# Performance work log

Hardware: AMD Instinct MI355X
Metric: run time of the kernel (lower is better)

## Reference

```python
import jax, jax.numpy as jnp
import numpy as np

# dims
C = 256; G = 16; GC = C // G; K = 3; P = K * K
N, H, W = 8, 56, 56
HID = int(C * 4.0)
PAD = 1; STRIDE = 1; DIL = 1
OFFSET_SCALE = 1.0
LN_EPS = 1e-6


def setup_inputs() -> dict:
    key = jax.random.key(0)
    ks = jax.random.split(key, 16)
    rn = lambda k, shape, s: jax.random.normal(k, shape, jnp.float32) * s
    return {
        "x": rn(ks[0], (N, H, W, C), 1.0),
        "norm1_g": jnp.ones((C,), jnp.float32), "norm1_b": jnp.zeros((C,), jnp.float32),
        "norm2_g": jnp.ones((C,), jnp.float32), "norm2_b": jnp.zeros((C,), jnp.float32),
        "gamma1": jnp.ones((C,), jnp.float32), "gamma2": jnp.ones((C,), jnp.float32),
        "dw_w": rn(ks[1], (C, 1, K, K), 0.1), "dw_b": rn(ks[2], (C,), 0.02),
        "dwln_g": jnp.ones((C,), jnp.float32), "dwln_b": jnp.zeros((C,), jnp.float32),
        "off_w": rn(ks[3], (C, G * P * 2), 0.01), "off_b": rn(ks[4], (G * P * 2,), 0.01),
        "mask_w": rn(ks[5], (C, G * P), 0.02), "mask_b": rn(ks[6], (G * P,), 0.02),
        "in_w": rn(ks[7], (C, C), C ** -0.5), "in_b": jnp.zeros((C,), jnp.float32),
        "out_w": rn(ks[8], (C, C), C ** -0.5), "out_b": jnp.zeros((C,), jnp.float32),
        "fc1_w": rn(ks[9], (C, HID), C ** -0.5), "fc1_b": jnp.zeros((HID,), jnp.float32),
        "fc2_w": rn(ks[10], (HID, C), HID ** -0.5), "fc2_b": jnp.zeros((C,), jnp.float32),
    }


def layer_norm(x, g, b):
    mu = x.mean(-1, keepdims=True)
    var = ((x - mu) ** 2).mean(-1, keepdims=True)
    return (x - mu) * jax.lax.rsqrt(var + LN_EPS) * g + b


def depthwise_conv(x, w, b):
    # x: (N,H,W,C), w: (C,1,K,K) depthwise
    y = jax.lax.conv_general_dilated(
        x.transpose(0, 3, 1, 2), w, (1, 1), ((PAD, PAD), (PAD, PAD)),
        feature_group_count=C)
    return y.transpose(0, 2, 3, 1) + b


def bilinear_gather(img, gx, gy):
    # img: (Hp,Wp,GC); gx,gy: (L,) normalized grid coords in [-1,1]
    # F.grid_sample(mode='bilinear', padding_mode='zeros', align_corners=False)
    Hp, Wp = img.shape[0], img.shape[1]
    x = (gx + 1.0) * 0.5 * Wp - 0.5
    y = (gy + 1.0) * 0.5 * Hp - 0.5
    x0 = jnp.floor(x); y0 = jnp.floor(y)
    lx = x - x0; ly = y - y0

    def tap(yi, xi, wgt):
        valid = (yi >= 0) & (yi < Hp) & (xi >= 0) & (xi < Wp)
        yc = jnp.clip(yi, 0, Hp - 1).astype(jnp.int32)
        xc = jnp.clip(xi, 0, Wp - 1).astype(jnp.int32)
        return jnp.where(valid, wgt, 0.0)[:, None] * img[yc, xc]  # (L,GC)

    return (tap(y0, x0, (1 - lx) * (1 - ly)) + tap(y0, x0 + 1, lx * (1 - ly))
            + tap(y0 + 1, x0, (1 - lx) * ly) + tap(y0 + 1, x0 + 1, lx * ly))


def dcnv3(xin, dw_w, dw_b, dwln_g, dwln_b, off_w, off_b, mask_w, mask_b,
          in_w, in_b, out_w, out_b):
    # xin: (N,H,W,C)
    xproj = xin @ in_w + in_b
    x1 = depthwise_conv(xin, dw_w, dw_b)
    x1 = jax.nn.gelu(layer_norm(x1, dwln_g, dwln_b), approximate=False)
    offset = x1 @ off_w + off_b                                   # (N,H,W,G*P*2)
    mask = jax.nn.softmax((x1 @ mask_w + mask_b).reshape(N, H, W, G, P), axis=-1)

    xp = jnp.pad(xproj, ((0, 0), (PAD, PAD), (PAD, PAD), (0, 0)))
    Hp, Wp = H + 2 * PAD, W + 2 * PAD

    # reference points, normalized by padded spatial shape; last dim = (x,y)
    base = (DIL * (K - 1)) // 2 + 0.5
    ref_y = (base + jnp.arange(H, dtype=jnp.float32) * STRIDE) / Hp
    ref_x = (base + jnp.arange(W, dtype=jnp.float32) * STRIDE) / Wp
    ref = jnp.stack(jnp.broadcast_arrays(ref_x[None, :], ref_y[:, None]), -1)  # (H,W,2)

    # dilation grid, x-major flatten order (torch meshgrid 'ij' on (x,y))
    lin = -float((DIL * (K - 1)) // 2) + jnp.arange(K, dtype=jnp.float32) * DIL
    gx, gy = jnp.meshgrid(lin, lin, indexing='ij')  # gx varies along dim0
    gridpts = jnp.stack([gx / Wp, gy / Hp], -1).reshape(P, 2)

    off = offset.reshape(N, H, W, G, P, 2) * OFFSET_SCALE / jnp.array([Wp, Hp], jnp.float32)
    loc = (ref[None, :, :, None, None, :] + gridpts[None, None, None, None, :, :] * OFFSET_SCALE
           + off)                                                 # (N,H,W,G,P,2)
    sg = 2.0 * loc - 1.0

    # per-group images and sampling grids
    img = xp.reshape(N, Hp, Wp, G, GC).transpose(0, 3, 1, 2, 4).reshape(N * G, Hp, Wp, GC)
    gxs = sg[..., 0].transpose(0, 3, 1, 2, 4).reshape(N * G, H * W * P)
    gys = sg[..., 1].transpose(0, 3, 1, 2, 4).reshape(N * G, H * W * P)
    sampled = jax.vmap(bilinear_gather)(img, gxs, gys)            # (N*G, H*W*P, GC)
    sampled = sampled.reshape(N, G, H, W, P, GC)

    out = jnp.einsum('nghwpc,nhwgp->nhwgc', sampled, mask).reshape(N, H, W, C)
    return out @ out_w + out_b


def reference(x, norm1_g, norm1_b, norm2_g, norm2_b, gamma1, gamma2,
              dw_w, dw_b, dwln_g, dwln_b, off_w, off_b, mask_w, mask_b,
              in_w, in_b, out_w, out_b, fc1_w, fc1_b, fc2_w, fc2_b):
    h = dcnv3(layer_norm(x, norm1_g, norm1_b), dw_w, dw_b, dwln_g, dwln_b,
              off_w, off_b, mask_w, mask_b, in_w, in_b, out_w, out_b)
    x = x + gamma1 * h
    m = jax.nn.gelu(layer_norm(x, norm2_g, norm2_b) @ fc1_w + fc1_b,
                    approximate=False) @ fc2_w + fc2_b
    return x + gamma2 * m
```

## Files before the change

kernel.cpp:

```cpp
#include <hip/hip_runtime.h>
#include <math.h>

#define NB 8
#define HH 56
#define WWD 56
#define CC 256
#define PIX (NB*HH*WWD)

typedef __attribute__((ext_vector_type(8))) short bf16x8;
typedef __attribute__((ext_vector_type(8))) unsigned short u16x8;
typedef __attribute__((ext_vector_type(4))) float f32x4;

__device__ __forceinline__ float gelu_fast(float x) {
    float z = x * fmaf(0.0713554668f, x*x, 1.5957691216f);
    return x * __fdividef(1.0f, 1.0f + __expf(-z));
}
__device__ __forceinline__ unsigned short f2bf(float f) {
    unsigned u = __float_as_uint(f);
    unsigned r = (u + 0x7fffu + ((u >> 16) & 1u)) >> 16;
    return (unsigned short)r;
}
__device__ __forceinline__ float bf2f(unsigned short b) {
    return __uint_as_float(((unsigned)b) << 16);
}
__device__ __forceinline__ void gl_lds16(const void* g, void* l) {
    __builtin_amdgcn_global_load_lds(
        (const __attribute__((address_space(1))) void*)g,
        (__attribute__((address_space(3))) void*)l, 16, 0, 0);
}
__device__ __forceinline__ void wave_reduce2(float& s, float& sq) {
    #pragma unroll
    for (int o = 32; o >= 1; o >>= 1) {
        s  += __shfl_xor(s, o);
        sq += __shfl_xor(sq, o);
    }
}

__global__ __launch_bounds__(256) void prep_kernel(
    const float* __restrict__ inw, const float* __restrict__ offw,
    const float* __restrict__ offb, const float* __restrict__ mskw,
    const float* __restrict__ mskb, const float* __restrict__ outw,
    const float* __restrict__ f1w, const float* __restrict__ f2w,
    const float* __restrict__ dww,
    unsigned short* __restrict__ bt_in, unsigned short* __restrict__ bt_om,
    unsigned short* __restrict__ bt_out, unsigned short* __restrict__ bt_fc1,
    unsigned short* __restrict__ bt_fc2, float* __restrict__ wt9,
    float* __restrict__ bias_om)
{
    int i = blockIdx.x * 256 + threadIdx.x;
    if (i < 65536) {
        int n = i >> 8, k = i & 255;
        bt_in[i] = f2bf(inw[(size_t)k*256 + n]);
    } else if (i < 196608) {
        int j = i - 65536;
        int n = j >> 8, k = j & 255;
        float v = (n < 288) ? offw[(size_t)k*288 + n]
                : (n < 432) ? mskw[(size_t)k*144 + (n-288)] : 0.f;
        bt_om[j] = f2bf(v);
    } else if (i < 262144) {
        int j = i - 196608;
        int n = j >> 8, k = j & 255;
        bt_out[j] = f2bf(outw[(size_t)k*256 + n]);
    } else if (i < 524288) {
        int j = i - 262144;
        int n = j >> 8, k = j & 255;
        bt_fc1[j] = f2bf(f1w[(size_t)k*1024 + n]);
    } else if (i < 786432) {
        int j = i - 524288;
        int n = j >> 10, k = j & 1023;
        bt_fc2[j] = f2bf(f2w[(size_t)k*256 + n]);
    } else if (i < 788736) {
        int j = i - 786432;
        int t = j >> 8, c = j & 255;
        wt9[j] = dww[(size_t)c*9 + t];
    } else if (i < 789248) {
        int j = i - 788736;
        bias_om[j] = (j < 288) ? offb[j] : (j < 432) ? mskb[j-288] : 0.f;
    }
}

__global__ __launch_bounds__(256) void ln_bf_kernel(
    const float* __restrict__ in, const float* __restrict__ g,
    const float* __restrict__ b, unsigned short* __restrict__ out)
{
    int wave = threadIdx.x >> 6, lane = threadIdx.x & 63;
    int pix = blockIdx.x * 4 + wave;
    int c0 = lane * 4;
    float4 v = *reinterpret_cast<const float4*>(&in[(size_t)pix * CC + c0]);
    float s = v.x + v.y + v.z + v.w;
    float sq = v.x*v.x + v.y*v.y + v.z*v.z + v.w*v.w;
    wave_reduce2(s, sq);
    float mu = s * (1.0f/256.0f);
    float var = sq * (1.0f/256.0f) - mu*mu;
    float rs = rsqrtf(var + 1e-6f);
    float4 gv = *reinterpret_cast<const float4*>(&g[c0]);
    float4 bv = *reinterpret_cast<const float4*>(&b[c0]);
    ushort4 o;
    o.x = f2bf((v.x-mu)*rs*gv.x + bv.x);
    o.y = f2bf((v.y-mu)*rs*gv.y + bv.y);
    o.z = f2bf((v.z-mu)*rs*gv.z + bv.z);
    o.w = f2bf((v.w-mu)*rs*gv.w + bv.w);
    *reinterpret_cast<ushort4*>(&out[(size_t)pix * CC + c0]) = o;
}

__global__ __launch_bounds__(256) void dwconv_ln_gelu_kernel(
    const unsigned short* __restrict__ xl, const float* __restrict__ wt9,
    const float* __restrict__ cb, const float* __restrict__ lg,
    const float* __restrict__ lb, unsigned short* __restrict__ out)
{
    int bid = blockIdx.x;
    int wg = (bid & 7) * (gridDim.x >> 3) + (bid >> 3);
    int wave = threadIdx.x >> 6, lane = threadIdx.x & 63;
    int pix0 = wg * 16 + wave * 4;
    int n = pix0 / (HH*WWD); int rem = pix0 % (HH*WWD);
    int h = rem / WWD, wb = rem % WWD;
    int c0 = lane * 4;

    float4 wv[9];
    #pragma unroll
    for (int t = 0; t < 9; ++t)
        wv[t] = *reinterpret_cast<const float4*>(&wt9[t*256 + c0]);
    float4 cbv = *reinterpret_cast<const float4*>(&cb[c0]);
    float4 gv  = *reinterpret_cast<const float4*>(&lg[c0]);
    float4 bv  = *reinterpret_cast<const float4*>(&lb[c0]);

    float4 a[4];
    #pragma unroll
    for (int px = 0; px < 4; ++px) a[px] = cbv;

    #pragma unroll
    for (int r = 0; r < 3; ++r) {
        int hh = h + r - 1;
        if (hh < 0 || hh >= HH) continue;
        const unsigned short* rowp = xl + (((size_t)n*HH + hh)*WWD)*CC + c0;
        #pragma unroll
        for (int dc = 0; dc < 6; ++dc) {
            int cc = wb - 1 + dc;
            if (cc < 0 || cc >= WWD) continue;
            ushort4 xv = *reinterpret_cast<const ushort4*>(&rowp[(size_t)cc*CC]);
            float fx = bf2f(xv.x), fy = bf2f(xv.y), fz = bf2f(xv.z), fw = bf2f(xv.w);
            #pragma unroll
            for (int px = 0; px < 4; ++px) {
                int kx = dc - px;
                if (kx >= 0 && kx < 3) {
                    float4 wq = wv[r*3 + kx];
                    a[px].x += fx*wq.x; a[px].y += fy*wq.y;
                    a[px].z += fz*wq.z; a[px].w += fw*wq.w;
                }
            }
        }
    }

    #pragma unroll
    for (int px = 0; px < 4; ++px) {
        float s = a[px].x + a[px].y + a[px].z + a[px].w;
        float sq = a[px].x*a[px].x + a[px].y*a[px].y + a[px].z*a[px].z + a[px].w*a[px].w;
        wave_reduce2(s, sq);
        float mu = s*(1.f/256.f), var = sq*(1.f/256.f) - mu*mu;
        float rs = rsqrtf(var + 1e-6f);
        ushort4 o;
        o.x = f2bf(gelu_fast((a[px].x-mu)*rs*gv.x + bv.x));
        o.y = f2bf(gelu_fast((a[px].y-mu)*rs*gv.y + bv.y));
        o.z = f2bf(gelu_fast((a[px].z-mu)*rs*gv.z + bv.z));
        o.w = f2bf(gelu_fast((a[px].w-mu)*rs*gv.w + bv.w));
        *reinterpret_cast<ushort4*>(&out[(size_t)(pix0+px)*CC + c0]) = o;
    }
}

template<int EPI>
__global__ __launch_bounds__(256, 4) void gemm_v4(
    const unsigned short* __restrict__ A, const unsigned short* __restrict__ Bt,
    const float* __restrict__ bias, float* __restrict__ Cf, float* __restrict__ Cf2,
    unsigned short* __restrict__ Cb, int M, int N, int K,
    const float* __restrict__ extra1, const float* __restrict__ extra2,
    const float* __restrict__ lng, const float* __restrict__ lnb)
{
    __shared__ unsigned short Al[16384];
    __shared__ float S1[4][64], S2[4][64];
    const int tid = threadIdx.x;
    const int wave = tid >> 6, lane = tid & 63;
    const int lm = lane & 15, kq = lane >> 4;

    int bid = blockIdx.x + blockIdx.y * gridDim.x;
    int nwg = gridDim.x * gridDim.y;
    int wg = (bid & 7) * (nwg >> 3) + (bid >> 3);
    const int m0 = (wg / gridDim.x) * 64;
    const int n0 = (wg % gridDim.x) * 256;
    const int n0w = n0 + wave * 64;

    f32x4 acc[4][4];
    #pragma unroll
    for (int i = 0; i < 4; ++i)
        #pragma unroll
        for (int j = 0; j < 4; ++j)
            acc[i][j] = (f32x4){0.f, 0.f, 0.f, 0.f};

    const unsigned short* Bw = Bt + (size_t)(n0w + lm) * K;

    const int nch = K >> 8;
    for (int ch = 0; ch < nch; ++ch) {
        if (ch) __syncthreads();
        int kc = ch << 8;
        #pragma unroll
        for (int jr = 0; jr < 8; ++jr) {
            int idx = jr*256 + tid;
            int kb = idx >> 6, row = idx & 63;
            gl_lds16(A + (size_t)(m0+row)*K + kc + kb*8,
                     (char*)Al + (jr*4 + wave)*1024);
        }
        __syncthreads();
        #pragma unroll
        for (int ks = 0; ks < 8; ++ks) {
            int kb = ks*4 + kq;
            bf16x8 af[4], bf[4];
            #pragma unroll
            for (int mi = 0; mi < 4; ++mi)
                af[mi] = *reinterpret_cast<const bf16x8*>(
                    &Al[(kb*64 + mi*16 + lm)*8]);
            #pragma unroll
            for (int ni = 0; ni < 4; ++ni)
                bf[ni] = *reinterpret_cast<const bf16x8*>(
                    &Bw[(size_t)ni*16*K + kc + ks*32 + kq*8]);
            #pragma unroll
            for (int mi = 0; mi < 4; ++mi)
                #pragma unroll
                for (int ni = 0; ni < 4; ++ni)
                    acc[mi][ni] = __builtin_amdgcn_mfma_f32_16x16x32_bf16(
                        af[mi], bf[ni], acc[mi][ni], 0, 0, 0);
        }
    }

    if (EPI == 5) {
        #pragma unroll
        for (int mi = 0; mi < 4; ++mi) {
            #pragma unroll
            for (int j = 0; j < 4; ++j) {
                int r = m0 + mi*16 + kq*4 + j;
                float ps = 0.f, pq = 0.f;
                #pragma unroll
                for (int ni = 0; ni < 4; ++ni) {
                    int c = n0w + ni*16 + lm;
                    float v = acc[mi][ni][j] + bias[c];
                    float xr = extra1[(size_t)r*N + c] + extra2[c]*v;
                    acc[mi][ni][j] = xr;
                    ps += xr; pq += xr*xr;
                }
                #pragma unroll
                for (int o = 8; o >= 1; o >>= 1) {
                    ps += __shfl_xor(ps, o);
                    pq += __shfl_xor(pq, o);
                }
                if (lm == 0) {
                    S1[wave][mi*16 + kq*4 + j] = ps;
                    S2[wave][mi*16 + kq*4 + j] = pq;
                }
            }
        }
        __syncthreads();
        #pragma unroll
        for (int mi = 0; mi < 4; ++mi) {
            #pragma unroll
            for (int j = 0; j < 4; ++j) {
                int rl = mi*16 + kq*4 + j;
                int r = m0 + rl;
                float s = S1[0][rl] + S1[1][rl] + S1[2][rl] + S1[3][rl];
                float sq = S2[0][rl] + S2[1][rl] + S2[2][rl] + S2[3][rl];
                float mu = s*(1.f/256.f), var = sq*(1.f/256.f) - mu*mu;
                float rs = rsqrtf(var + 1e-6f);
                #pragma unroll
                for (int ni = 0; ni < 4; ++ni) {
                    int c = n0w + ni*16 + lm;
                    float xr = acc[mi][ni][j];
                    Cf[(size_t)r*N + c] = xr;
                    Cb[(size_t)r*N + c] = f2bf((xr-mu)*rs*lng[c] + lnb[c]);
                }
            }
        }
        return;
    }

    #pragma unroll
    for (int mi = 0; mi < 4; ++mi) {
        #pragma unroll
        for (int ni = 0; ni < 4; ++ni) {
            int c = n0w + ni*16 + lm;
            float bb = bias[c];
            #pragma unroll
            for (int j = 0; j < 4; ++j) {
                int r = m0 + mi*16 + kq*4 + j;
                float v = acc[mi][ni][j] + bb;
                if (EPI == 1) {
                    Cb[(size_t)r*N + c] = f2bf(gelu_fast(v));
                } else if (EPI == 2) {
                    size_t gi = (size_t)r*N + c;
                    Cf[gi] = extra1[gi] + extra2[c]*v;
                } else if (EPI == 3) {
                    Cb[(size_t)r*N + c] = f2bf(v);
                } else if (EPI == 4) {
                    if (c < 288)
                        ((unsigned short*)Cf)[(size_t)r*288 + c] = f2bf(v);
                    else if (c < 432)
                        ((unsigned short*)Cf2)[(size_t)r*144 + (c-288)] = f2bf(v);
                }
            }
        }
    }
}

__device__ __forceinline__ void tap8(const unsigned short* __restrict__ img, int yi, int xi,
                                     float wgt, float* s) {
    if (yi >= 1 && yi <= 56 && xi >= 1 && xi <= 56) {
        u16x8 v = *reinterpret_cast<const u16x8*>(
            &img[(((size_t)(yi-1))*WWD + (xi-1)) * CC]);
        #pragma unroll
        for (int k = 0; k < 8; ++k) s[k] += wgt*bf2f(v[k]);
    }
}

__global__ __launch_bounds__(256) void dcn_sample_kernel(
    const unsigned short* __restrict__ xproj, const unsigned short* __restrict__ offs,
    const unsigned short* __restrict__ msk, unsigned short* __restrict__ dcn)
{
    int bid = blockIdx.x;
    int wg = (bid & 7) * (gridDim.x >> 3) + (bid >> 3);
    int wave = threadIdx.x >> 6, lane = threadIdx.x & 63;
    int px = lane >> 5, g = (lane >> 1) & 15, c8 = lane & 1;
    int pix = wg * 8 + wave * 2 + px;
    int n = pix / (HH*WWD); int rem = pix % (HH*WWD);
    int h = rem / WWD, w = rem % WWD;
    const unsigned short* op = offs + (size_t)pix*288 + g*18;
    const unsigned short* mp = msk + (size_t)pix*144 + g*9;
    const unsigned short* img = xproj + (size_t)n*(HH*WWD*CC) + g*16 + c8*8;

    float mv[9]; float mx = -1e30f;
    #pragma unroll
    for (int j = 0; j < 9; ++j) { mv[j] = bf2f(mp[j]); mx = fmaxf(mx, mv[j]); }
    float ssum = 0.f;
    #pragma unroll
    for (int j = 0; j < 9; ++j) { mv[j] = __expf(mv[j]-mx); ssum += mv[j]; }
    float minv = __fdividef(1.f, ssum);

    float acc[8] = {0.f,0.f,0.f,0.f,0.f,0.f,0.f,0.f};
    #pragma unroll
    for (int p = 0; p < 9; ++p) {
        ushort2 o2 = *reinterpret_cast<const ushort2*>(&op[p*2]);
        float ox = bf2f(o2.x), oy = bf2f(o2.y);
        float xs = (float)(w + p/3) + ox;
        float ys = (float)(h + p%3) + oy;
        float x0f = floorf(xs), y0f = floorf(ys);
        float lx = xs - x0f, ly = ys - y0f;
        int x0 = (int)x0f, y0 = (int)y0f;
        float s[8] = {0.f,0.f,0.f,0.f,0.f,0.f,0.f,0.f};
        tap8(img, y0,   x0,   (1.f-lx)*(1.f-ly), s);
        tap8(img, y0,   x0+1, lx*(1.f-ly),       s);
        tap8(img, y0+1, x0,   (1.f-lx)*ly,       s);
        tap8(img, y0+1, x0+1, lx*ly,             s);
        float m = mv[p]*minv;
        #pragma unroll
        for (int k = 0; k < 8; ++k) acc[k] += m*s[k];
    }
    u16x8 o;
    #pragma unroll
    for (int k = 0; k < 8; ++k) o[k] = f2bf(acc[k]);
    *reinterpret_cast<u16x8*>(&dcn[(size_t)pix*CC + g*16 + c8*8]) = o;
}

extern "C" void kernel_launch(void* const* d_in, const int* in_sizes, int n_in,
                              void* d_out, int out_size, void* d_ws, size_t ws_size,
                              hipStream_t stream)
{
    const float* x    = (const float*)d_in[0];
    const float* n1g  = (const float*)d_in[1];
    const float* n1b  = (const float*)d_in[2];
    const float* n2g  = (const float*)d_in[3];
    const float* n2b  = (const float*)d_in[4];
    const float* g1   = (const float*)d_in[5];
    const float* g2   = (const float*)d_in[6];
    const float* dww  = (const float*)d_in[7];
    const float* dwb  = (const float*)d_in[8];
    const float* dlng = (const float*)d_in[9];
    const float* dlnb = (const float*)d_in[10];
    const float* offw = (const float*)d_in[11];
    const float* offb = (const float*)d_in[12];
    const float* mskw = (const float*)d_in[13];
    const float* mskb = (const float*)d_in[14];
    const float* inw  = (const float*)d_in[15];
    const float* inb  = (const float*)d_in[16];
    const float* outw = (const float*)d_in[17];
    const float* outb = (const float*)d_in[18];
    const float* f1w  = (const float*)d_in[19];
    const float* f1b  = (const float*)d_in[20];
    const float* f2w  = (const float*)d_in[21];
    const float* f2b  = (const float*)d_in[22];
    float* out = (float*)d_out;

    char* base = (char*)d_ws;
    unsigned short* xl_bf    = (unsigned short*)(base + 0);
    unsigned short* xproj_bf = (unsigned short*)(base + 12845056);
    float*          xres     = (float*)(base + 25690112);
    unsigned short* x1_bf    = (unsigned short*)(base + 51380224);
    unsigned short* offs_bf  = (unsigned short*)(base + 64225280);
    unsigned short* msk_bf   = (unsigned short*)(base + 78675968);
    unsigned short* dcn_bf   = xl_bf;
    unsigned short* y2_bf    = x1_bf;
    unsigned short* h1       = (unsigned short*)(base + 64225280 + 21676032);
    unsigned short* btb      = (unsigned short*)(base + 64225280 + 21676032 + 51380224);
    unsigned short* bt_in  = btb + 0;
    unsigned short* bt_om  = btb + 65536;
    unsigned short* bt_out = btb + 196608;
    unsigned short* bt_fc1 = btb + 262144;
    unsigned short* bt_fc2 = btb + 524288;
    float*          wt9     = (float*)(btb + 786432);
    float*          bias_om = (float*)(btb + 805888);

    prep_kernel<<<3084, 256, 0, stream>>>(inw, offw, offb, mskw, mskb, outw,
        f1w, f2w, dww, bt_in, bt_om, bt_out, bt_fc1, bt_fc2, wt9, bias_om);

    ln_bf_kernel<<<PIX/4, 256, 0, stream>>>(x, n1g, n1b, xl_bf);
    gemm_v4<3><<<dim3(1,392), 256, 0, stream>>>(xl_bf, bt_in, inb, nullptr, nullptr,
        xproj_bf, PIX, 256, 256, nullptr, nullptr, nullptr, nullptr);
    dwconv_ln_gelu_kernel<<<PIX/16, 256, 0, stream>>>(xl_bf, wt9, dwb, dlng, dlnb, x1_bf);
    gemm_v4<4><<<dim3(2,392), 256, 0, stream>>>(x1_bf, bt_om, bias_om,
        (float*)offs_bf, (float*)msk_bf, nullptr, PIX, 512, 256,
        nullptr, nullptr, nullptr, nullptr);
    dcn_sample_kernel<<<PIX/8, 256, 0, stream>>>(xproj_bf, offs_bf, msk_bf, dcn_bf);
    gemm_v4<5><<<dim3(1,392), 256, 0, stream>>>(dcn_bf, bt_out, outb, xres, nullptr,
        y2_bf, PIX, 256, 256, x, g1, n2g, n2b);
    gemm_v4<1><<<dim3(4,392), 256, 0, stream>>>(y2_bf, bt_fc1, f1b, nullptr, nullptr,
        h1, PIX, 1024, 256, nullptr, nullptr, nullptr, nullptr);
    gemm_v4<2><<<dim3(1,392), 256, 0, stream>>>(h1, bt_fc2, f2b, out, nullptr,
        nullptr, PIX, 256, 1024, xres, g2, nullptr, nullptr);
}
```

Measured before the change: 233.2 us.

## Merge independent stages into combined launches and split MLP in halves for overlap

Independent stages now share one launch, with blocks dispatched by block index: weight prep runs alongside LN1, and the input projection GEMM alongside the depthwise conv. The MLP is split into two row halves so the second half of fc1 can run in the same launch as the first half of fc2, and the second half of fc2 runs last. This is meant to cut launch gaps and tail idling by overlapping work with different resource needs. It moves shared memory to dynamic allocation and adds a guard so the XCD swizzle only applies when the block count is a multiple of eight.

```diff
diff --git a/kernel.cpp b/kernel.cpp
--- a/kernel.cpp
+++ b/kernel.cpp
@@ -6,6 +6,7 @@
 #define WWD 56
 #define CC 256
 #define PIX (NB*HH*WWD)
+#define HALF (PIX/2)
 
 typedef __attribute__((ext_vector_type(8))) short bf16x8;
 typedef __attribute__((ext_vector_type(8))) unsigned short u16x8;
@@ -35,8 +36,12 @@
         sq += __shfl_xor(sq, o);
     }
 }
-
-__global__ __launch_bounds__(256) void prep_kernel(
+__device__ __forceinline__ int xcd_swz(int bid, int nwg) {
+    return (nwg & 7) ? bid : (bid & 7) * (nwg >> 3) + (bid >> 3);
+}
+
+
+__device__ void prep_dev(int b,
     const float* __restrict__ inw, const float* __restrict__ offw,
     const float* __restrict__ offb, const float* __restrict__ mskw,
     const float* __restrict__ mskb, const float* __restrict__ outw,
@@ -47,7 +52,7 @@
     unsigned short* __restrict__ bt_fc2, float* __restrict__ wt9,
     float* __restrict__ bias_om)
 {
-    int i = blockIdx.x * 256 + threadIdx.x;
+    int i = b * 256 + threadIdx.x;
     if (i < 65536) {
         int n = i >> 8, k = i & 255;
         bt_in[i] = f2bf(inw[(size_t)k*256 + n]);
@@ -79,12 +84,12 @@
     }
 }
 
-__global__ __launch_bounds__(256) void ln_bf_kernel(
-    const float* __restrict__ in, const float* __restrict__ g,
-    const float* __restrict__ b, unsigned short* __restrict__ out)
+__device__ void ln_dev(int b, const float* __restrict__ in,
+    const float* __restrict__ g, const float* __restrict__ bb,
+    unsigned short* __restrict__ out)
 {
     int wave = threadIdx.x >> 6, lane = threadIdx.x & 63;
-    int pix = blockIdx.x * 4 + wave;
+    int pix = b * 4 + wave;
     int c0 = lane * 4;
     float4 v = *reinterpret_cast<const float4*>(&in[(size_t)pix * CC + c0]);
     float s = v.x + v.y + v.z + v.w;
@@ -94,7 +99,7 @@
     float var = sq * (1.0f/256.0f) - mu*mu;
     float rs = rsqrtf(var + 1e-6f);
     float4 gv = *reinterpret_cast<const float4*>(&g[c0]);
-    float4 bv = *reinterpret_cast<const float4*>(&b[c0]);
+    float4 bv = *reinterpret_cast<const float4*>(&bb[c0]);
     ushort4 o;
     o.x = f2bf((v.x-mu)*rs*gv.x + bv.x);
     o.y = f2bf((v.y-mu)*rs*gv.y + bv.y);
@@ -103,13 +108,12 @@
     *reinterpret_cast<ushort4*>(&out[(size_t)pix * CC + c0]) = o;
 }
 
-__global__ __launch_bounds__(256) void dwconv_ln_gelu_kernel(
+__device__ void dwconv_dev(int bid, int nwg,
     const unsigned short* __restrict__ xl, const float* __restrict__ wt9,
     const float* __restrict__ cb, const float* __restrict__ lg,
     const float* __restrict__ lb, unsigned short* __restrict__ out)
 {
-    int bid = blockIdx.x;
-    int wg = (bid & 7) * (gridDim.x >> 3) + (bid >> 3);
+    int wg = xcd_swz(bid, nwg);
     int wave = threadIdx.x >> 6, lane = threadIdx.x & 63;
     int pix0 = wg * 16 + wave * 4;
     int n = pix0 / (HH*WWD); int rem = pix0 % (HH*WWD);
@@ -168,24 +172,23 @@
 }
 
 template<int EPI>
-__global__ __launch_bounds__(256, 4) void gemm_v4(
+__device__ void gemm_dev(char* smem, int bid, int nwg, int gridX,
     const unsigned short* __restrict__ A, const unsigned short* __restrict__ Bt,
     const float* __restrict__ bias, float* __restrict__ Cf, float* __restrict__ Cf2,
-    unsigned short* __restrict__ Cb, int M, int N, int K,
+    unsigned short* __restrict__ Cb, int N, int K,
     const float* __restrict__ extra1, const float* __restrict__ extra2,
     const float* __restrict__ lng, const float* __restrict__ lnb)
 {
-    __shared__ unsigned short Al[16384];
-    __shared__ float S1[4][64], S2[4][64];
+    unsigned short* Al = (unsigned short*)smem;
+    float* S1 = (float*)(smem + 32768);
+    float* S2 = (float*)(smem + 32768 + 1024);
     const int tid = threadIdx.x;
     const int wave = tid >> 6, lane = tid & 63;
     const int lm = lane & 15, kq = lane >> 4;
 
-    int bid = blockIdx.x + blockIdx.y * gridDim.x;
-    int nwg = gridDim.x * gridDim.y;
-    int wg = (bid & 7) * (nwg >> 3) + (bid >> 3);
-    const int m0 = (wg / gridDim.x) * 64;
-    const int n0 = (wg % gridDim.x) * 256;
+    int wg = xcd_swz(bid, nwg);
+    const int m0 = (wg / gridX) * 64;
+    const int n0 = (wg % gridX) * 256;
     const int n0w = n0 + wave * 64;
 
     f32x4 acc[4][4];
@@ -206,7 +209,7 @@
             int idx = jr*256 + tid;
             int kb = idx >> 6, row = idx & 63;
             gl_lds16(A + (size_t)(m0+row)*K + kc + kb*8,
-                     (char*)Al + (jr*4 + wave)*1024);
+                     smem + (jr*4 + wave)*1024);
         }
         __syncthreads();
         #pragma unroll
@@ -251,8 +254,8 @@
                     pq += __shfl_xor(pq, o);
                 }
                 if (lm == 0) {
-                    S1[wave][mi*16 + kq*4 + j] = ps;
-                    S2[wave][mi*16 + kq*4 + j] = pq;
+                    S1[wave*64 + mi*16 + kq*4 + j] = ps;
+                    S2[wave*64 + mi*16 + kq*4 + j] = pq;
                 }
             }
         }
@@ -263,8 +266,8 @@
             for (int j = 0; j < 4; ++j) {
                 int rl = mi*16 + kq*4 + j;
                 int r = m0 + rl;
-                float s = S1[0][rl] + S1[1][rl] + S1[2][rl] + S1[3][rl];
-                float sq = S2[0][rl] + S2[1][rl] + S2[2][rl] + S2[3][rl];
+                float s = S1[rl] + S1[64+rl] + S1[128+rl] + S1[192+rl];
+                float sq = S2[rl] + S2[64+rl] + S2[128+rl] + S2[192+rl];
                 float mu = s*(1.f/256.f), var = sq*(1.f/256.f) - mu*mu;
                 float rs = rsqrtf(var + 1e-6f);
                 #pragma unroll
@@ -307,6 +310,92 @@
     }
 }
 
+
+__global__ __launch_bounds__(256) void k_prep_ln(
+    const float* inw, const float* offw, const float* offb, const float* mskw,
+    const float* mskb, const float* outw, const float* f1w, const float* f2w,
+    const float* dww, unsigned short* bt_in, unsigned short* bt_om,
+    unsigned short* bt_out, unsigned short* bt_fc1, unsigned short* bt_fc2,
+    float* wt9, float* bias_om,
+    const float* x, const float* n1g, const float* n1b, unsigned short* xl)
+{
+    int b = blockIdx.x;
+    if (b < 3084)
+        prep_dev(b, inw, offw, offb, mskw, mskb, outw, f1w, f2w, dww,
+                 bt_in, bt_om, bt_out, bt_fc1, bt_fc2, wt9, bias_om);
+    else
+        ln_dev(b - 3084, x, n1g, n1b, xl);
+}
+
+__global__ __launch_bounds__(256, 4) void k_inproj_dw(
+    const unsigned short* xl, const unsigned short* bt_in, const float* inb,
+    unsigned short* xproj, const float* wt9, const float* dwb,
+    const float* dlng, const float* dlnb, unsigned short* x1)
+{
+    extern __shared__ char smem[];
+    int b = blockIdx.x;
+    if (b < 392)
+        gemm_dev<3>(smem, b, 392, 1, xl, bt_in, inb, nullptr, nullptr, xproj,
+                    256, 256, nullptr, nullptr, nullptr, nullptr);
+    else
+        dwconv_dev(b - 392, 1568, xl, wt9, dwb, dlng, dlnb, x1);
+}
+
+__global__ __launch_bounds__(256, 4) void k_om(
+    const unsigned short* x1, const unsigned short* bt_om, const float* bias_om,
+    unsigned short* offs, unsigned short* msk)
+{
+    extern __shared__ char smem[];
+    gemm_dev<4>(smem, blockIdx.x, 784, 2, x1, bt_om, bias_om,
+                (float*)offs, (float*)msk, nullptr, 512, 256,
+                nullptr, nullptr, nullptr, nullptr);
+}
+
+__global__ __launch_bounds__(256, 4) void k_outproj(
+    const unsigned short* dcn, const unsigned short* bt_out, const float* outb,
+    float* xres, unsigned short* y2, const float* x, const float* g1,
+    const float* n2g, const float* n2b)
+{
+    extern __shared__ char smem[];
+    gemm_dev<5>(smem, blockIdx.x, 392, 1, dcn, bt_out, outb, xres, nullptr, y2,
+                256, 256, x, g1, n2g, n2b);
+}
+
+__global__ __launch_bounds__(256, 4) void k_fc1a(
+    const unsigned short* y2, const unsigned short* bt_fc1, const float* f1b,
+    unsigned short* h1)
+{
+    extern __shared__ char smem[];
+    gemm_dev<1>(smem, blockIdx.x, 784, 4, y2, bt_fc1, f1b, nullptr, nullptr, h1,
+                1024, 256, nullptr, nullptr, nullptr, nullptr);
+}
+
+__global__ __launch_bounds__(256, 4) void k_fc1b_fc2a(
+    const unsigned short* y2, const unsigned short* bt_fc1, const float* f1b,
+    unsigned short* h1, const unsigned short* bt_fc2, const float* f2b,
+    float* out, const float* xres, const float* g2)
+{
+    extern __shared__ char smem[];
+    int b = blockIdx.x;
+    if (b < 784)
+        gemm_dev<1>(smem, b, 784, 4, y2 + (size_t)HALF*256, bt_fc1, f1b,
+                    nullptr, nullptr, h1 + (size_t)HALF*1024,
+                    1024, 256, nullptr, nullptr, nullptr, nullptr);
+    else
+        gemm_dev<2>(smem, b - 784, 196, 1, h1, bt_fc2, f2b, out, nullptr,
+                    nullptr, 256, 1024, xres, g2, nullptr, nullptr);
+}
+
+__global__ __launch_bounds__(256, 4) void k_fc2b(
+    const unsigned short* h1, const unsigned short* bt_fc2, const float* f2b,
+    float* out, const float* xres, const float* g2)
+{
+    extern __shared__ char smem[];
+    gemm_dev<2>(smem, blockIdx.x, 196, 1, h1 + (size_t)HALF*1024, bt_fc2, f2b,
+                out + (size_t)HALF*256, nullptr, nullptr, 256, 1024,
+                xres + (size_t)HALF*256, g2, nullptr, nullptr);
+}
+
 __device__ __forceinline__ void tap8(const unsigned short* __restrict__ img, int yi, int xi,
                                      float wgt, float* s) {
     if (yi >= 1 && yi <= 56 && xi >= 1 && xi <= 56) {
@@ -321,8 +410,7 @@
     const unsigned short* __restrict__ xproj, const unsigned short* __restrict__ offs,
     const unsigned short* __restrict__ msk, unsigned short* __restrict__ dcn)
 {
-    int bid = blockIdx.x;
-    int wg = (bid & 7) * (gridDim.x >> 3) + (bid >> 3);
+    int wg = xcd_swz(blockIdx.x, gridDim.x);
     int wave = threadIdx.x >> 6, lane = threadIdx.x & 63;
     int px = lane >> 5, g = (lane >> 1) & 15, c8 = lane & 1;
     int pix = wg * 8 + wave * 2 + px;
@@ -413,21 +501,20 @@
     float*          wt9     = (float*)(btb + 786432);
     float*          bias_om = (float*)(btb + 805888);
 
-    prep_kernel<<<3084, 256, 0, stream>>>(inw, offw, offb, mskw, mskb, outw,
-        f1w, f2w, dww, bt_in, bt_om, bt_out, bt_fc1, bt_fc2, wt9, bias_om);
-
-    ln_bf_kernel<<<PIX/4, 256, 0, stream>>>(x, n1g, n1b, xl_bf);
-    gemm_v4<3><<<dim3(1,392), 256, 0, stream>>>(xl_bf, bt_in, inb, nullptr, nullptr,
-        xproj_bf, PIX, 256, 256, nullptr, nullptr, nullptr, nullptr);
-    dwconv_ln_gelu_kernel<<<PIX/16, 256, 0, stream>>>(xl_bf, wt9, dwb, dlng, dlnb, x1_bf);
-    gemm_v4<4><<<dim3(2,392), 256, 0, stream>>>(x1_bf, bt_om, bias_om,
-        (float*)offs_bf, (float*)msk_bf, nullptr, PIX, 512, 256,
-        nullptr, nullptr, nullptr, nullptr);
+    const size_t SM  = 32768;
+    const size_t SM5 = 32768 + 2048;
+
+    k_prep_ln<<<9356, 256, 0, stream>>>(inw, offw, offb, mskw, mskb, outw,
+        f1w, f2w, dww, bt_in, bt_om, bt_out, bt_fc1, bt_fc2, wt9, bias_om,
+        x, n1g, n1b, xl_bf);
+    k_inproj_dw<<<1960, 256, SM, stream>>>(xl_bf, bt_in, inb, xproj_bf,
+        wt9, dwb, dlng, dlnb, x1_bf);
+    k_om<<<784, 256, SM, stream>>>(x1_bf, bt_om, bias_om, offs_bf, msk_bf);
     dcn_sample_kernel<<<PIX/8, 256, 0, stream>>>(xproj_bf, offs_bf, msk_bf, dcn_bf);
-    gemm_v4<5><<<dim3(1,392), 256, 0, stream>>>(dcn_bf, bt_out, outb, xres, nullptr,
-        y2_bf, PIX, 256, 256, x, g1, n2g, n2b);
-    gemm_v4<1><<<dim3(4,392), 256, 0, stream>>>(y2_bf, bt_fc1, f1b, nullptr, nullptr,
-        h1, PIX, 1024, 256, nullptr, nullptr, nullptr, nullptr);
-    gemm_v4<2><<<dim3(1,392), 256, 0, stream>>>(h1, bt_fc2, f2b, out, nullptr,
-        nullptr, PIX, 256, 1024, xres, g2, nullptr, nullptr);
-}
+    k_outproj<<<392, 256, SM5, stream>>>(dcn_bf, bt_out, outb, xres, y2_bf,
+        x, g1, n2g, n2b);
+    k_fc1a<<<784, 256, SM, stream>>>(y2_bf, bt_fc1, f1b, h1);
+    k_fc1b_fc2a<<<980, 256, SM, stream>>>(y2_bf, bt_fc1, f1b, h1,
+        bt_fc2, f2b, out, xres, g2);
+    k_fc2b<<<196, 256, SM, stream>>>(h1, bt_fc2, f2b, out, xres, g2);
+}
```

New measurement: 263.1 us. 12.8% more time.
